# Kernel tuning notes

Measured on AMD Instinct MI355X. Metric: run time of the kernel, lower is better.

Reference implementation:

```python
import jax, jax.numpy as jnp
import numpy as np

N = 100_000      # nodes
E = 1_600_000    # edges (avg degree 16)
H = 2            # heads
C = 32           # out channels per head
L = 4            # EGAT layers
IN = 4           # input one-hot dim (node labels)
ECLS = 5         # edge classes (ratings)
SCALE = 0.1


def setup_inputs() -> dict:
    key = jax.random.key(0)
    ks = jax.random.split(key, 8)
    # node labels arange%4 -> equal user (0) / item (1) counts; x is one-hot (input_embedding=False)
    labels = jnp.arange(N) % 4
    x = jax.nn.one_hot(labels, IN, dtype=jnp.float32)
    edge_index = jax.random.randint(ks[0], (2, E), 0, N)
    edge_attr = jax.random.randint(ks[1], (E,), 0, ECLS)
    W0 = jax.random.normal(ks[2], (IN, H * C), dtype=jnp.float32) * SCALE
    W13 = jax.random.normal(ks[3], (L - 1, H * C, H * C), dtype=jnp.float32) * SCALE
    eemb = jax.random.normal(ks[4], (L, ECLS, H * C), dtype=jnp.float32) * SCALE
    att_src = jax.random.normal(ks[5], (L, H, C), dtype=jnp.float32) * SCALE
    att_dst = jax.random.normal(ks[6], (L, H, C), dtype=jnp.float32) * SCALE
    bias = jnp.zeros((L, H * C), dtype=jnp.float32)
    return dict(x=x, W0=W0, W13=W13, eemb=eemb, att_src=att_src,
                att_dst=att_dst, bias=bias, edge_index=edge_index, edge_attr=edge_attr)


def _egat_layer(x, W, eemb_l, a_src, a_dst, b, src, dst, edge_attr):
    # x: [N, Fin] -> h: [N, H, C]
    h = (x @ W).reshape(N, H, C)
    e = eemb_l[edge_attr].reshape(E, H, C)            # per-edge type embedding
    m = h[src] + e                                    # [E, H, C] edge-featured message
    logits = jax.nn.leaky_relu(
        jnp.sum(h[dst] * a_dst, axis=-1) + jnp.sum(m * a_src, axis=-1), 0.2)  # [E, H]
    # ragged softmax over incoming edges of each destination node
    amax = jax.ops.segment_max(logits, dst, num_segments=N)
    amax = jnp.where(jnp.isfinite(amax), amax, 0.0)
    ex = jnp.exp(logits - amax[dst])
    denom = jax.ops.segment_sum(ex, dst, num_segments=N)
    alpha = ex / (denom[dst] + 1e-16)                 # [E, H]
    out = jax.ops.segment_sum(alpha[..., None] * m, dst, num_segments=N)  # [N, H, C]
    return jax.nn.elu(out.reshape(N, H * C) + b)      # concat heads + elu activation


def reference(x, W0, W13, eemb, att_src, att_dst, bias, edge_index, edge_attr):
    src, dst = edge_index[0], edge_index[1]
    h = _egat_layer(x, W0, eemb[0], att_src[0], att_dst[0], bias[0], src, dst, edge_attr)
    for l in range(1, L):
        h = _egat_layer(h, W13[l - 1], eemb[l], att_src[l], att_dst[l], bias[l], src, dst, edge_attr)
    # users are nodes with label 0 (x[:,0]==1), items label 1 (x[:,1]==1);
    # labels were built as arange(N)%4, so user/item indices are static strided slices.
    user_idx = jnp.arange(0, N, 4)
    item_idx = jnp.arange(1, N, 4)
    u = h[user_idx]
    v = h[item_idx]
    return jnp.sum(u * v, axis=-1)  # MF decoder, multiply_by=1
```

## Files before the change

kernel.cpp:

```cpp
#include <hip/hip_runtime.h>
#include <hip/hip_bf16.h>
#include <math.h>

#define N_NODES 100000
#define N_EDGES 1600000
#define HC 64
#define NHEADS 2
#define NLAYERS 4
#define ECLS 5
#define NBUCK 196
#define NBLK 512
#define EPB (N_EDGES / NBLK)
#define NGRP (N_NODES / 16)
#define LIN0_BLOCKS 1024
#define FCAP 12288
#define CHS 68

typedef __attribute__((ext_vector_type(8))) short short8;
typedef __attribute__((ext_vector_type(4))) float floatx4;
union F8 { uint4 u; short8 s; };

__device__ inline float bf_lo(unsigned int u) { return __uint_as_float(u << 16); }
__device__ inline float bf_hi(unsigned int u) { return __uint_as_float(u & 0xffff0000u); }
__device__ inline unsigned short f2bf(float f) {
    unsigned int u = __float_as_uint(f);
    u += 0x7FFFu + ((u >> 16) & 1u);
    return (unsigned short)(u >> 16);
}

__global__ void k_chist_lin0(const int* __restrict__ dst, int* __restrict__ bh,
                             const float* __restrict__ in,
                             const float* __restrict__ W,
                             const float* __restrict__ asrc, const float* __restrict__ adst,
                             unsigned short* __restrict__ hcurb,
                             float* __restrict__ ssrc, float* __restrict__ sdst,
                             const float* __restrict__ eemb, float* __restrict__ escore) {
    int tid = threadIdx.x;
    if (blockIdx.x < NBLK) {
        __shared__ int lh[NBUCK];
        int blk = blockIdx.x;
        for (int i = tid; i < NBUCK; i += 256) lh[i] = 0;
        __syncthreads();
        int s = blk * EPB;
        for (int i = tid; i < EPB; i += 256) atomicAdd(&lh[dst[s + i] >> 9], 1);
        __syncthreads();
        for (int i = tid; i < NBUCK; i += 256) bh[i * NBLK + blk] = lh[i];
        return;
    }
    if (blockIdx.x >= NBLK + LIN0_BLOCKS) {
        if (tid < NLAYERS * ECLS * NHEADS) {
            int l = tid / (ECLS * NHEADS);
            int r = tid % (ECLS * NHEADS);
            int c = r >> 1;
            int h = r & 1;
            float s = 0.f;
            const float* ev = eemb + l * ECLS * HC + c * HC + h * 32;
            const float* av = asrc + l * HC + h * 32;
            for (int k = 0; k < 32; ++k) s += ev[k] * av[k];
            escore[tid] = s;
        }
        return;
    }
    int j = tid & 63;
    int wid = ((blockIdx.x - NBLK) * 256 + tid) >> 6;
    int nwaves = LIN0_BLOCKS * 4;

    float w0 = W[0 * HC + j], w1 = W[1 * HC + j], w2 = W[2 * HC + j], w3 = W[3 * HC + j];
    int head = j >> 5;
    int c = j & 31;
    float as = asrc[head * 32 + c];
    float ad = adst[head * 32 + c];

    for (int n = wid; n < N_NODES; n += nwaves) {
        int nu = __builtin_amdgcn_readfirstlane(n);
        float4 r = *(const float4*)(in + (size_t)nu * 4);
        float acc = r.x * w0 + r.y * w1 + r.z * w2 + r.w * w3;
        hcurb[(size_t)nu * HC + j] = f2bf(acc);
        float ps = acc * as;
        float pd = acc * ad;
        for (int off = 16; off > 0; off >>= 1) {
            ps += __shfl_down(ps, off, 32);
            pd += __shfl_down(pd, off, 32);
        }
        if (c == 0) {
            ssrc[nu * 2 + head] = ps;
            sdst[nu * 2 + head] = pd;
        }
    }
}

__global__ void k_s1(const int* __restrict__ bh, int* __restrict__ bbase,
                     int* __restrict__ part) {
    __shared__ int tmp[NBLK];
    int tid = threadIdx.x;
    int i = blockIdx.x * NBLK + tid;
    int v = bh[i];
    tmp[tid] = v;
    __syncthreads();
    for (int off = 1; off < NBLK; off <<= 1) {
        int t = (tid >= off) ? tmp[tid - off] : 0;
        __syncthreads();
        tmp[tid] += t;
        __syncthreads();
    }
    bbase[i] = tmp[tid] - v;
    if (tid == NBLK - 1) part[blockIdx.x] = tmp[NBLK - 1];
}

__global__ void k_cscatter(const int* __restrict__ src, const int* __restrict__ dst,
                           const int* __restrict__ attr, const int* __restrict__ bbase,
                           const int* __restrict__ part, int* __restrict__ bkt) {
    __shared__ int tmp[256];
    __shared__ int cur[NBUCK];
    __shared__ int gadj[NBUCK];
    __shared__ int stage[EPB];
    __shared__ unsigned char stb[EPB];
    int tid = threadIdx.x, blk = blockIdx.x;
    int pv = (tid < NBUCK) ? part[tid] : 0;
    tmp[tid] = pv;
    __syncthreads();
    for (int off = 1; off < 256; off <<= 1) {
        int t = (tid >= off) ? tmp[tid - off] : 0;
        __syncthreads();
        tmp[tid] += t;
        __syncthreads();
    }
    if (tid < NBUCK) gadj[tid] = tmp[tid] - pv;
    if (tid < NBUCK) cur[tid] = 0;
    for (int i = tid + 256; i < NBUCK; i += 256) cur[i] = 0;
    __syncthreads();
    int s0 = blk * EPB;
    for (int i = tid; i < EPB; i += 256) atomicAdd(&cur[dst[s0 + i] >> 9], 1);
    __syncthreads();
    int v = (tid < NBUCK) ? cur[tid] : 0;
    tmp[tid] = v;
    __syncthreads();
    for (int off = 1; off < 256; off <<= 1) {
        int t = (tid >= off) ? tmp[tid - off] : 0;
        __syncthreads();
        tmp[tid] += t;
        __syncthreads();
    }
    int ex = tmp[tid] - v;
    if (tid < NBUCK) {
        cur[tid] = ex;
        gadj[tid] += bbase[tid * NBLK + blk] - ex;
    }
    __syncthreads();
    for (int i = tid; i < EPB; i += 256) {
        int e = s0 + i;
        int d = dst[e];
        int b = d >> 9;
        int pos = atomicAdd(&cur[b], 1);
        stage[pos] = src[e] | (attr[e] << 17) | ((d & 511) << 20);
        stb[pos] = (unsigned char)b;
    }
    __syncthreads();
    for (int i = tid; i < EPB; i += 256)
        bkt[gadj[stb[i]] + i] = stage[i];
}

__global__ void k_fine(const int* __restrict__ part, const int* __restrict__ bkt,
                       int* __restrict__ packed, int* __restrict__ rowstart) {
    __shared__ int hist[512];
    __shared__ int cur[512];
    __shared__ int pscan[512];
    __shared__ int stage[FCAP];
    int b = blockIdx.x, tid = threadIdx.x;
    int pv = (tid < NBUCK) ? part[tid] : 0;
    pscan[tid] = pv;
    __syncthreads();
    for (int off = 1; off < 512; off <<= 1) {
        int t = (tid >= off) ? pscan[tid - off] : 0;
        __syncthreads();
        pscan[tid] += t;
        __syncthreads();
    }
    int base = (b == 0) ? 0 : pscan[b - 1];
    int bend = pscan[b];
    int nb = bend - base;
    hist[tid] = 0;
    __syncthreads();
    for (int i = tid; i < nb; i += 512)
        atomicAdd(&hist[(bkt[base + i] >> 20) & 0x1FF], 1);
    __syncthreads();
    int v = hist[tid];
    for (int off = 1; off < 512; off <<= 1) {
        int t = (tid >= off) ? hist[tid - off] : 0;
        __syncthreads();
        hist[tid] += t;
        __syncthreads();
    }
    int excl = hist[tid] - v;
    int node = (b << 9) + tid;
    if (node <= N_NODES) rowstart[node] = base + excl;
    cur[tid] = excl;
    __syncthreads();
    if (nb <= FCAP) {
        for (int i = tid; i < nb; i += 512) {
            int p = bkt[base + i];
            int r = atomicAdd(&cur[(p >> 20) & 0x1FF], 1);
            stage[r] = p;
        }
        __syncthreads();
        for (int i = tid; i < nb; i += 512) packed[base + i] = stage[i];
    } else {
        for (int i = tid; i < nb; i += 512) {
            int p = bkt[base + i];
            int r = atomicAdd(&cur[(p >> 20) & 0x1FF], 1);
            packed[base + r] = p;
        }
    }
}

__global__ void k_linmfma(const unsigned short* __restrict__ actB,
                          const float* __restrict__ Wl,
                          const float* __restrict__ asrc,
                          const float* __restrict__ adst,
                          unsigned short* __restrict__ hcurb,
                          float* __restrict__ ssrc, float* __restrict__ sdst) {
    __shared__ uint4 WB[512];
    __shared__ unsigned short Cb[4][1024];
    int tid = threadIdx.x;
    int lane = tid & 63;
    int w = tid >> 6;
    int q = lane >> 4;
    int c = lane & 15;

    for (int rid = tid; rid < 512; rid += 256) {
        int kk = rid >> 8;
        int t  = (rid >> 6) & 3;
        int ln = rid & 63;
        int qq = ln >> 4, cc = ln & 15;
        unsigned int u[4];
        #pragma unroll
        for (int jj = 0; jj < 4; ++jj) {
            float v0 = Wl[(kk * 32 + qq * 8 + jj * 2 + 0) * 64 + 16 * t + cc];
            float v1 = Wl[(kk * 32 + qq * 8 + jj * 2 + 1) * 64 + 16 * t + cc];
            u[jj] = (unsigned int)f2bf(v0) | ((unsigned int)f2bf(v1) << 16);
        }
        WB[rid] = make_uint4(u[0], u[1], u[2], u[3]);
    }
    __syncthreads();

    short8 bfr[2][4];
    #pragma unroll
    for (int kk = 0; kk < 2; ++kk)
        #pragma unroll
        for (int t = 0; t < 4; ++t) {
            F8 tmp; tmp.u = WB[(kk * 4 + t) * 64 + lane];
            bfr[kk][t] = tmp.s;
        }

    float as_[4], ad_[4];
    #pragma unroll
    for (int t = 0; t < 4; ++t) {
        as_[t] = asrc[16 * t + c];
        ad_[t] = adst[16 * t + c];
    }

    int wid = (blockIdx.x * 256 + tid) >> 6;
    int nwaves = gridDim.x * 4;

    for (int g = wid; g < NGRP; g += nwaves) {
        int base = g * 16;
        F8 a0, a1;
        a0.u = *(const uint4*)(actB + (size_t)(base + c) * HC + q * 8);
        a1.u = *(const uint4*)(actB + (size_t)(base + c) * HC + 32 + q * 8);

        floatx4 acc[4];
        #pragma unroll
        for (int t = 0; t < 4; ++t) {
            acc[t] = (floatx4){0.f, 0.f, 0.f, 0.f};
            acc[t] = __builtin_amdgcn_mfma_f32_16x16x32_bf16(a0.s, bfr[0][t], acc[t], 0, 0, 0);
            acc[t] = __builtin_amdgcn_mfma_f32_16x16x32_bf16(a1.s, bfr[1][t], acc[t], 0, 0, 0);
        }

        #pragma unroll
        for (int r = 0; r < 4; ++r) {
            float h0s = acc[0][r] * as_[0] + acc[1][r] * as_[1];
            float h1s = acc[2][r] * as_[2] + acc[3][r] * as_[3];
            float h0d = acc[0][r] * ad_[0] + acc[1][r] * ad_[1];
            float h1d = acc[2][r] * ad_[2] + acc[3][r] * ad_[3];
            #pragma unroll
            for (int off = 1; off < 16; off <<= 1) {
                h0s += __shfl_xor(h0s, off, 64);
                h1s += __shfl_xor(h1s, off, 64);
                h0d += __shfl_xor(h0d, off, 64);
                h1d += __shfl_xor(h1d, off, 64);
            }
            if (c == 0) {
                int node = base + q * 4 + r;
                *(float2*)(ssrc + node * 2) = make_float2(h0s, h1s);
                *(float2*)(sdst + node * 2) = make_float2(h0d, h1d);
            }
        }

        #pragma unroll
        for (int t = 0; t < 4; ++t)
            #pragma unroll
            for (int r = 0; r < 4; ++r)
                Cb[w][(q * 4 + r) * 64 + 16 * t + c] = f2bf(acc[t][r]);
        __builtin_amdgcn_wave_barrier();
        const uint4* cf = (const uint4*)&Cb[w][0];
        uint4* gout = (uint4*)(hcurb + (size_t)base * HC);
        gout[lane] = cf[lane];
        gout[64 + lane] = cf[64 + lane];
        __builtin_amdgcn_wave_barrier();
    }
}

template <int NW, bool LAST>
__global__ void k_edge(const int* __restrict__ rowstart, const int* __restrict__ packed,
                       const float* __restrict__ ssrc, const float* __restrict__ sdst,
                       const float* __restrict__ escore_l,
                       const unsigned short* __restrict__ hcurb,
                       const float* __restrict__ eemb_l,
                       const float* __restrict__ bias_l,
                       unsigned short* __restrict__ actnext, float* __restrict__ out) {
    __shared__ float chbuf[NW][8 * CHS];
    __shared__ float obuf[2][64];
    int w = threadIdx.x >> 6;
    int n = LAST ? (blockIdx.x * 4 + w) : (blockIdx.x * NW + w);
    int lane = threadIdx.x & 63;
    int sub = lane >> 3;
    int q   = lane & 7;
    int h   = q >> 2;

    int beg = rowstart[n];
    int end = rowstart[n + 1];
    float sd = sdst[n * 2 + h];

    float4 a0 = make_float4(0.f, 0.f, 0.f, 0.f);
    float4 a1 = make_float4(0.f, 0.f, 0.f, 0.f);
    float ssum = 0.f;
    for (int i = beg + sub; i < end; i += 8) {
        int p = packed[i];
        int s = p & 0x1FFFF;
        int a = (p >> 17) & 7;
        float lg = sd + ssrc[s * 2 + h] + escore_l[a * 2 + h];
        lg = lg >= 0.f ? lg : 0.2f * lg;
        float wt = __expf(lg);
        uint4 hv = *(const uint4*)(hcurb + (size_t)s * HC + q * 8);
        const float4* ep = (const float4*)(eemb_l + a * HC + q * 8);
        float4 e0 = ep[0], e1 = ep[1];
        a0.x += wt * (bf_lo(hv.x) + e0.x);
        a0.y += wt * (bf_hi(hv.x) + e0.y);
        a0.z += wt * (bf_lo(hv.y) + e0.z);
        a0.w += wt * (bf_hi(hv.y) + e0.w);
        a1.x += wt * (bf_lo(hv.z) + e1.x);
        a1.y += wt * (bf_hi(hv.z) + e1.y);
        a1.z += wt * (bf_lo(hv.w) + e1.z);
        a1.w += wt * (bf_hi(hv.w) + e1.w);
        ssum += wt;
    }
    ((float4*)&chbuf[w][sub * CHS + q * 8])[0] = a0;
    ((float4*)&chbuf[w][sub * CHS + q * 8])[1] = a1;
    for (int off = 8; off < 64; off <<= 1) ssum += __shfl_xor(ssum, off, 64);
    float ssum_h = __shfl(ssum, (lane >> 5) * 4, 64);
    float inv = 1.f / (ssum_h + 1e-16f);
    __builtin_amdgcn_wave_barrier();
    float s = 0.f;
    #pragma unroll
    for (int k = 0; k < 8; ++k) s += chbuf[w][k * CHS + lane];
    float v = s * inv + bias_l[lane];
    float o = v > 0.f ? v : (__expf(v) - 1.f);
    if (!LAST) {
        actnext[(size_t)n * HC + lane] = f2bf(o);
    } else {
        obuf[w][lane] = o;
        __syncthreads();
        if (w == 0) {
            float p = obuf[0][lane] * obuf[1][lane];
            for (int off = 32; off > 0; off >>= 1) p += __shfl_down(p, off, 64);
            if (lane == 0) out[blockIdx.x] = p;
        }
    }
}

extern "C" void kernel_launch(void* const* d_in, const int* in_sizes, int n_in,
                              void* d_out, int out_size, void* d_ws, size_t ws_size,
                              hipStream_t stream) {
    const float* x       = (const float*)d_in[0];
    const float* W0      = (const float*)d_in[1];
    const float* W13     = (const float*)d_in[2];
    const float* eemb    = (const float*)d_in[3];
    const float* att_src = (const float*)d_in[4];
    const float* att_dst = (const float*)d_in[5];
    const float* bias    = (const float*)d_in[6];
    const int*   eidx    = (const int*)d_in[7];
    const int*   eattr   = (const int*)d_in[8];
    float* out = (float*)d_out;

    const int* src = eidx;
    const int* dst = eidx + N_EDGES;

    char* wsb = (char*)d_ws;
    size_t off = 0;
    auto alloc = [&](size_t bytes) { char* p = wsb + off; off += (bytes + 255) & ~(size_t)255; return p; };
    unsigned short* hcurb  = (unsigned short*)alloc((size_t)N_NODES * HC * 2);
    unsigned short* actB   = (unsigned short*)alloc((size_t)N_NODES * HC * 2);
    float*          ssrc   = (float*)alloc((size_t)N_NODES * 2 * 4);
    float*          sdst   = (float*)alloc((size_t)N_NODES * 2 * 4);
    float*          escore = (float*)alloc(NLAYERS * ECLS * NHEADS * 4);
    int*            bh     = (int*)alloc((size_t)NBUCK * NBLK * 4);
    int*            bbase  = (int*)alloc((size_t)NBUCK * NBLK * 4);
    int*            part   = (int*)alloc(256 * 4);
    int*            rowstart = (int*)alloc(((size_t)N_NODES + 1) * 4);
    int*            bkt    = (int*)alloc((size_t)N_EDGES * 4);
    int*            packed = (int*)alloc((size_t)N_EDGES * 4);

    k_chist_lin0<<<NBLK + LIN0_BLOCKS + 1, 256, 0, stream>>>(
        dst, bh, x, W0, att_src, att_dst, hcurb, ssrc, sdst, eemb, escore);
    k_s1<<<NBUCK, NBLK, 0, stream>>>(bh, bbase, part);
    k_cscatter<<<NBLK, 256, 0, stream>>>(src, dst, eattr, bbase, part, bkt);
    k_fine<<<NBUCK, 512, 0, stream>>>(part, bkt, packed, rowstart);

    for (int l = 0; l < NLAYERS; ++l) {
        if (l > 0) {
            k_linmfma<<<512, 256, 0, stream>>>(
                actB, W13 + (size_t)(l - 1) * HC * HC,
                att_src + l * HC, att_dst + l * HC, hcurb, ssrc, sdst);
        }
        const float* esl = escore + l * ECLS * NHEADS;
        const float* el  = eemb + (size_t)l * ECLS * HC;
        const float* bl  = bias + l * HC;
        if (l < NLAYERS - 1)
            k_edge<1, false><<<N_NODES, 64, 0, stream>>>(
                rowstart, packed, ssrc, sdst, esl, hcurb, el, bl, actB, nullptr);
        else
            k_edge<2, true><<<N_NODES / 4, 128, 0, stream>>>(
                rowstart, packed, ssrc, sdst, esl, hcurb, el, bl, nullptr, out);
    }
}
```

Before: 319.9 us.

## Restructure edge aggregation with per-span attention precompute and class-summed edge embeddings

Replaces the one-wave-per-node edge kernel with a block that handles a span of 32 or 64 destination nodes. The block first computes both heads' attention weights for all edges in the span into shared memory, and accumulates per-class weight sums with LDS atomics. Edge embeddings are then applied once per class (the sum of weight times embedding over edge classes) instead of being loaded per edge. Each 8-lane group walks its node's edges serially, two at a time, and the last layer computes the user-item dot product with shuffles. This removes the per-edge eemb loads, the cross-subgroup LDS reduction and duplicated exp work, at the cost of shared-memory atomics, load imbalance across nodes of different degree, and a fallback path when edges exceed the shared-memory buffer.

```diff
diff --git a/kernel.cpp b/kernel.cpp
--- a/kernel.cpp
+++ b/kernel.cpp
@@ -4,6 +4,7 @@
 
 #define N_NODES 100000
 #define N_EDGES 1600000
+#define NPAIRS 25000
 #define HC 64
 #define NHEADS 2
 #define NLAYERS 4
@@ -14,7 +15,6 @@
 #define NGRP (N_NODES / 16)
 #define LIN0_BLOCKS 1024
 #define FCAP 12288
-#define CHS 68
 
 typedef __attribute__((ext_vector_type(8))) short short8;
 typedef __attribute__((ext_vector_type(4))) float floatx4;
@@ -310,71 +310,165 @@
     }
 }
 
-template <int NW, bool LAST>
-__global__ void k_edge(const int* __restrict__ rowstart, const int* __restrict__ packed,
-                       const float* __restrict__ ssrc, const float* __restrict__ sdst,
-                       const float* __restrict__ escore_l,
-                       const unsigned short* __restrict__ hcurb,
-                       const float* __restrict__ eemb_l,
-                       const float* __restrict__ bias_l,
-                       unsigned short* __restrict__ actnext, float* __restrict__ out) {
-    __shared__ float chbuf[NW][8 * CHS];
-    __shared__ float obuf[2][64];
-    int w = threadIdx.x >> 6;
-    int n = LAST ? (blockIdx.x * 4 + w) : (blockIdx.x * NW + w);
-    int lane = threadIdx.x & 63;
-    int sub = lane >> 3;
-    int q   = lane & 7;
-    int h   = q >> 2;
-
-    int beg = rowstart[n];
-    int end = rowstart[n + 1];
-    float sd = sdst[n * 2 + h];
+template <bool LAST>
+__global__ __launch_bounds__(256)
+void k_edge2(const int* __restrict__ rowstart, const int* __restrict__ packed,
+             const float* __restrict__ ssrc, const float* __restrict__ sdst,
+             const float* __restrict__ escore_l,
+             const unsigned short* __restrict__ hcurb,
+             const float* __restrict__ eemb_l,
+             const float* __restrict__ bias_l,
+             unsigned short* __restrict__ actnext, float* __restrict__ out) {
+    constexpr int SPAN = LAST ? 64 : 32;
+    constexpr int CAP  = LAST ? 1440 : 800;
+    __shared__ float4 ebuf[CAP];
+    __shared__ float  cls[SPAN * 10];
+    __shared__ float2 sdl[SPAN];
+    __shared__ float2 esc2[ECLS];
+
+    const int tid = threadIdx.x;
+    const int n0 = blockIdx.x * SPAN;
+
+    for (int i = tid; i < SPAN * 10; i += 256) cls[i] = 0.f;
+    if (tid < ECLS) esc2[tid] = ((const float2*)escore_l)[tid];
+    if (tid < SPAN) {
+        int nn = n0 + tid; if (nn > N_NODES - 1) nn = N_NODES - 1;
+        sdl[tid] = ((const float2*)sdst)[nn];
+    }
+    int spanEnd = n0 + SPAN; if (spanEnd > N_NODES) spanEnd = N_NODES;
+    const int beg = rowstart[n0];
+    const int end = rowstart[spanEnd];
+    __syncthreads();
+
+    const int nb = end - beg;
+    for (int i = tid; i < nb; i += 256) {
+        int p = packed[beg + i];
+        int dl = ((p >> 20) & 511) - (n0 & 511);
+        if (!LAST || ((dl & 2) == 0)) {
+            int s = p & 0x1FFFF;
+            int a = (p >> 17) & 7;
+            float2 sv = *(const float2*)(ssrc + s * 2);
+            float2 dv = sdl[dl];
+            float2 ev = esc2[a];
+            float l0 = dv.x + sv.x + ev.x; l0 = l0 >= 0.f ? l0 : 0.2f * l0;
+            float l1 = dv.y + sv.y + ev.y; l1 = l1 >= 0.f ? l1 : 0.2f * l1;
+            float w0 = __expf(l0), w1 = __expf(l1);
+            if (i < CAP) ebuf[i] = make_float4(__int_as_float(p), w0, w1, 0.f);
+            atomicAdd(&cls[dl * 10 + a * 2 + 0], w0);
+            atomicAdd(&cls[dl * 10 + a * 2 + 1], w1);
+        }
+    }
+    __syncthreads();
+
+    const int lane = tid & 63;
+    const int q = lane & 7;
+    const int hh = q >> 2;
+    const int slot = (tid >> 6) * 8 + (lane >> 3);
+    int myn, pair = 0;
+    bool valid = true;
+    if (LAST) {
+        pair = blockIdx.x * 16 + (slot >> 1);
+        valid = pair < NPAIRS;
+        myn = n0 + (slot >> 1) * 4 + (slot & 1);
+    } else {
+        myn = n0 + slot;
+    }
+    const int b0 = valid ? rowstart[myn] : 0;
+    const int b1 = valid ? rowstart[myn + 1] : 0;
+    const unsigned short* hb = hcurb + q * 8;
 
     float4 a0 = make_float4(0.f, 0.f, 0.f, 0.f);
     float4 a1 = make_float4(0.f, 0.f, 0.f, 0.f);
+
+    struct PE { int p; float wt; };
+    auto fetch = [&](int i) -> PE {
+        PE r;
+        int j = i - beg;
+        if (j < CAP) {
+            float4 t = ebuf[j];
+            r.p = __float_as_int(t.x);
+            r.wt = hh ? t.z : t.y;
+        } else {
+            int p = packed[i];
+            int aa = (p >> 17) & 7;
+            int ss = p & 0x1FFFF;
+            int dll = ((p >> 20) & 511) - (n0 & 511);
+            float2 dv2 = sdl[dll];
+            float2 ev2 = esc2[aa];
+            float lg = (hh ? dv2.y : dv2.x) + ssrc[ss * 2 + hh] + (hh ? ev2.y : ev2.x);
+            lg = lg >= 0.f ? lg : 0.2f * lg;
+            r.p = p;
+            r.wt = __expf(lg);
+        }
+        return r;
+    };
+
+#define ACC8(wt, hv) do { \
+        a0.x += (wt) * bf_lo((hv).x); a0.y += (wt) * bf_hi((hv).x); \
+        a0.z += (wt) * bf_lo((hv).y); a0.w += (wt) * bf_hi((hv).y); \
+        a1.x += (wt) * bf_lo((hv).z); a1.y += (wt) * bf_hi((hv).z); \
+        a1.z += (wt) * bf_lo((hv).w); a1.w += (wt) * bf_hi((hv).w); \
+    } while (0)
+
+    int i = b0;
+    for (; i + 2 <= b1; i += 2) {
+        PE e0 = fetch(i);
+        PE e1 = fetch(i + 1);
+        uint4 h0 = *(const uint4*)(hb + ((e0.p & 0x1FFFF) << 6));
+        uint4 h1 = *(const uint4*)(hb + ((e1.p & 0x1FFFF) << 6));
+        ACC8(e0.wt, h0);
+        ACC8(e1.wt, h1);
+    }
+    if (i < b1) {
+        PE e0 = fetch(i);
+        uint4 h0 = *(const uint4*)(hb + ((e0.p & 0x1FFFF) << 6));
+        ACC8(e0.wt, h0);
+    }
+#undef ACC8
+
+    const int dl = myn - n0;
     float ssum = 0.f;
-    for (int i = beg + sub; i < end; i += 8) {
-        int p = packed[i];
-        int s = p & 0x1FFFF;
-        int a = (p >> 17) & 7;
-        float lg = sd + ssrc[s * 2 + h] + escore_l[a * 2 + h];
-        lg = lg >= 0.f ? lg : 0.2f * lg;
-        float wt = __expf(lg);
-        uint4 hv = *(const uint4*)(hcurb + (size_t)s * HC + q * 8);
-        const float4* ep = (const float4*)(eemb_l + a * HC + q * 8);
-        float4 e0 = ep[0], e1 = ep[1];
-        a0.x += wt * (bf_lo(hv.x) + e0.x);
-        a0.y += wt * (bf_hi(hv.x) + e0.y);
-        a0.z += wt * (bf_lo(hv.y) + e0.z);
-        a0.w += wt * (bf_hi(hv.y) + e0.w);
-        a1.x += wt * (bf_lo(hv.z) + e1.x);
-        a1.y += wt * (bf_hi(hv.z) + e1.y);
-        a1.z += wt * (bf_lo(hv.w) + e1.z);
-        a1.w += wt * (bf_hi(hv.w) + e1.w);
-        ssum += wt;
-    }
-    ((float4*)&chbuf[w][sub * CHS + q * 8])[0] = a0;
-    ((float4*)&chbuf[w][sub * CHS + q * 8])[1] = a1;
-    for (int off = 8; off < 64; off <<= 1) ssum += __shfl_xor(ssum, off, 64);
-    float ssum_h = __shfl(ssum, (lane >> 5) * 4, 64);
-    float inv = 1.f / (ssum_h + 1e-16f);
-    __builtin_amdgcn_wave_barrier();
-    float s = 0.f;
+    const float* ef = eemb_l + q * 8;
     #pragma unroll
-    for (int k = 0; k < 8; ++k) s += chbuf[w][k * CHS + lane];
-    float v = s * inv + bias_l[lane];
-    float o = v > 0.f ? v : (__expf(v) - 1.f);
+    for (int a = 0; a < ECLS; ++a) {
+        float c = cls[dl * 10 + a * 2 + hh];
+        ssum += c;
+        float4 e0 = *(const float4*)(ef + a * HC);
+        float4 e1 = *(const float4*)(ef + a * HC + 4);
+        a0.x += c * e0.x; a0.y += c * e0.y; a0.z += c * e0.z; a0.w += c * e0.w;
+        a1.x += c * e1.x; a1.y += c * e1.y; a1.z += c * e1.z; a1.w += c * e1.w;
+    }
+    float inv = 1.f / (ssum + 1e-16f);
+    float4 bv0 = *(const float4*)(bias_l + q * 8);
+    float4 bv1 = *(const float4*)(bias_l + q * 8 + 4);
+    float o0 = a0.x * inv + bv0.x; o0 = o0 > 0.f ? o0 : (__expf(o0) - 1.f);
+    float o1 = a0.y * inv + bv0.y; o1 = o1 > 0.f ? o1 : (__expf(o1) - 1.f);
+    float o2 = a0.z * inv + bv0.z; o2 = o2 > 0.f ? o2 : (__expf(o2) - 1.f);
+    float o3 = a0.w * inv + bv0.w; o3 = o3 > 0.f ? o3 : (__expf(o3) - 1.f);
+    float o4 = a1.x * inv + bv1.x; o4 = o4 > 0.f ? o4 : (__expf(o4) - 1.f);
+    float o5 = a1.y * inv + bv1.y; o5 = o5 > 0.f ? o5 : (__expf(o5) - 1.f);
+    float o6 = a1.z * inv + bv1.z; o6 = o6 > 0.f ? o6 : (__expf(o6) - 1.f);
+    float o7 = a1.w * inv + bv1.w; o7 = o7 > 0.f ? o7 : (__expf(o7) - 1.f);
+
     if (!LAST) {
-        actnext[(size_t)n * HC + lane] = f2bf(o);
+        unsigned int u0 = (unsigned int)f2bf(o0) | ((unsigned int)f2bf(o1) << 16);
+        unsigned int u1 = (unsigned int)f2bf(o2) | ((unsigned int)f2bf(o3) << 16);
+        unsigned int u2 = (unsigned int)f2bf(o4) | ((unsigned int)f2bf(o5) << 16);
+        unsigned int u3 = (unsigned int)f2bf(o6) | ((unsigned int)f2bf(o7) << 16);
+        *(uint4*)(actnext + (size_t)myn * HC + q * 8) = make_uint4(u0, u1, u2, u3);
     } else {
-        obuf[w][lane] = o;
-        __syncthreads();
-        if (w == 0) {
-            float p = obuf[0][lane] * obuf[1][lane];
-            for (int off = 32; off > 0; off >>= 1) p += __shfl_down(p, off, 64);
-            if (lane == 0) out[blockIdx.x] = p;
-        }
+        float pdot = o0 * __shfl_xor(o0, 8, 64)
+                   + o1 * __shfl_xor(o1, 8, 64)
+                   + o2 * __shfl_xor(o2, 8, 64)
+                   + o3 * __shfl_xor(o3, 8, 64)
+                   + o4 * __shfl_xor(o4, 8, 64)
+                   + o5 * __shfl_xor(o5, 8, 64)
+                   + o6 * __shfl_xor(o6, 8, 64)
+                   + o7 * __shfl_xor(o7, 8, 64);
+        pdot += __shfl_xor(pdot, 1, 64);
+        pdot += __shfl_xor(pdot, 2, 64);
+        pdot += __shfl_xor(pdot, 4, 64);
+        if (valid && ((slot & 1) == 0) && (q == 0)) out[pair] = pdot;
     }
 }
 
@@ -426,10 +520,10 @@
         const float* el  = eemb + (size_t)l * ECLS * HC;
         const float* bl  = bias + l * HC;
         if (l < NLAYERS - 1)
-            k_edge<1, false><<<N_NODES, 64, 0, stream>>>(
+            k_edge2<false><<<N_NODES / 32, 256, 0, stream>>>(
                 rowstart, packed, ssrc, sdst, esl, hcurb, el, bl, actB, nullptr);
         else
-            k_edge<2, true><<<N_NODES / 4, 128, 0, stream>>>(
+            k_edge2<true><<<(NPAIRS + 15) / 16, 256, 0, stream>>>(
                 rowstart, packed, ssrc, sdst, esl, hcurb, el, bl, nullptr, out);
     }
 }
```

After: 328.4 us. 2.6% more time.
